# Kernel tuning notes

Measured on AMD Instinct MI355X. Metric: run time of the kernel, lower is better.

The kernel has to match this reference:

```python
import jax, jax.numpy as jnp
import numpy as np

B, D, H, W, Q = 16, 768, 64, 64, 128


def setup_inputs() -> dict:
    key = jax.random.key(0)
    ks = jax.random.split(key, 6)
    s = 0.02  # param init scale
    return {
        "visual_feat": jax.random.normal(ks[0], (B, D, H, W), jnp.float32),
        "text_feat": jax.random.normal(ks[1], (B, Q, D), jnp.float32),
        "Wq": jax.random.normal(ks[2], (D, D), jnp.float32) * s,
        "bq": jnp.zeros((D,), jnp.float32),
        "Wk": jax.random.normal(ks[3], (D, D), jnp.float32) * s,
        "bk": jnp.zeros((D,), jnp.float32),
        "Wv": jax.random.normal(ks[4], (D, D), jnp.float32) * s,
        "bv": jnp.zeros((D,), jnp.float32),
    }


def _entropy_weights(x):
    # x: [B, T, D] -> softmax over features, per-token entropy, softmax over tokens -> [B, T]
    p = jax.nn.softmax(x, axis=-1)
    ent = -jnp.sum(p * jnp.log(p + 1e-9), axis=-1)
    return jax.nn.softmax(ent, axis=-1)


def reference(visual_feat, text_feat, Wq, bq, Wk, bk, Wv, bv):
    b, d, h, w = visual_feat.shape
    vf = visual_feat.reshape(b, d, h * w).transpose(0, 2, 1)  # [B, N, D]
    ve = _entropy_weights(vf)          # [B, N]
    te = _entropy_weights(text_feat)   # [B, Q]
    q = vf @ Wq.T + bq                 # [B, N, D]
    k = text_feat @ Wk.T + bk          # [B, Q, D]
    v = text_feat @ Wv.T + bv          # [B, Q, D]
    attn = jnp.einsum('bnd,bqd->bnq', q, k) / jnp.sqrt(jnp.float32(d))
    attn = attn * (ve[:, :, None] * te[:, None, :])  # entropy outer-product modulation
    attn = jax.nn.softmax(attn, axis=-1)
    enhanced = jnp.einsum('bnq,bqd->bnd', attn, v)   # [B, N, D]
    return enhanced.transpose(0, 2, 1).reshape(b, d, h, w)
```

## Files before the change

kernel.cpp:

```cpp
#include <hip/hip_runtime.h>

#define B_ 16
#define D_ 768
#define N_ 4096
#define Q_ 128

typedef __attribute__((ext_vector_type(4))) float f32x4;
typedef __attribute__((ext_vector_type(8))) short short8;
typedef __attribute__((ext_vector_type(4))) short sv4;

__device__ __forceinline__ unsigned short f2bf(float f) {
  union { float f; unsigned u; } x; x.f = f;
  unsigned u = x.u;
  unsigned r = u + 0x7fffu + ((u >> 16) & 1u);
  return (unsigned short)(r >> 16);
}
__device__ __forceinline__ float bf2f(unsigned short h) {
  union { unsigned u; float f; } x; x.u = ((unsigned)h) << 16;
  return x.f;
}

__global__ __launch_bounds__(256) void cast_bf16_kernel(
    const float* __restrict__ src, unsigned short* __restrict__ dst, int n4) {
  int i = blockIdx.x * 256 + threadIdx.x;
  if (i >= n4) return;
  float4 v = ((const float4*)src)[i];
  ushort4 o;
  o.x = f2bf(v.x); o.y = f2bf(v.y); o.z = f2bf(v.z); o.w = f2bf(v.w);
  ((ushort4*)dst)[i] = o;
}

__global__ __launch_bounds__(256) void transpose_cast_kernel(
    const float* __restrict__ src, unsigned short* __restrict__ dst, int rows, int cols) {
  __shared__ float tile[32][33];
  int bx = blockIdx.x * 32, by = blockIdx.y * 32;
  int tx = threadIdx.x & 31, ty = threadIdx.x >> 5;
  #pragma unroll
  for (int i = 0; i < 32; i += 8)
    tile[ty + i][tx] = src[(size_t)(by + ty + i) * cols + bx + tx];
  __syncthreads();
  #pragma unroll
  for (int i = 0; i < 32; i += 8)
    dst[(size_t)(bx + ty + i) * rows + by + tx] = f2bf(tile[tx][ty + i]);
}

__global__ __launch_bounds__(256) void row_entropy_kernel(
    const float* __restrict__ X, float* __restrict__ ent, int K) {
  int row = blockIdx.x * 4 + (threadIdx.x >> 6);
  int lane = threadIdx.x & 63;
  const float* x = X + (size_t)row * K;
  float m = -__builtin_inff(), s = 0.f, t = 0.f;
  for (int k = lane; k < K; k += 64) {
    float v = x[k];
    float nm = fmaxf(m, v);
    float c = __expf(m - nm);
    float e = __expf(v - nm);
    s = s * c + e;
    t = t * c + v * e;
    m = nm;
  }
  #pragma unroll
  for (int off = 32; off > 0; off >>= 1) {
    float m2 = __shfl_xor(m, off);
    float s2 = __shfl_xor(s, off);
    float t2 = __shfl_xor(t, off);
    float nm = fmaxf(m, m2);
    float c1 = __expf(m - nm), c2 = __expf(m2 - nm);
    s = s * c1 + s2 * c2;
    t = t * c1 + t2 * c2;
    m = nm;
  }
  if (lane == 0) ent[row] = m + __logf(s) - t / s;
}

__global__ __launch_bounds__(256) void visual_entropy_kernel(
    const float* __restrict__ vis, float* __restrict__ ent) {
  int bb = blockIdx.x >> 6;
  int n0 = (blockIdx.x & 63) * 64;
  int t = threadIdx.x;
  int tok = t & 63;
  int slice = t >> 6;
  const float* base = vis + (size_t)bb * D_ * N_ + (size_t)slice * 192 * N_ + n0 + tok;
  float m = -__builtin_inff(), s = 0.f, tt = 0.f;
  for (int d = 0; d < 192; d++) {
    float v = base[(size_t)d * N_];
    float nm = fmaxf(m, v);
    float c = __expf(m - nm);
    float e = __expf(v - nm);
    s = s * c + e; tt = tt * c + v * e; m = nm;
  }
  __shared__ float sm[256], ss[256], st[256];
  sm[t] = m; ss[t] = s; st[t] = tt;
  __syncthreads();
  if (t < 64) {
    #pragma unroll
    for (int k = 1; k < 4; k++) {
      float m2 = sm[t + 64 * k], s2 = ss[t + 64 * k], t2 = st[t + 64 * k];
      float nm = fmaxf(m, m2);
      float c1 = __expf(m - nm), c2 = __expf(m2 - nm);
      s = s * c1 + s2 * c2; tt = tt * c1 + t2 * c2; m = nm;
    }
    ent[(size_t)bb * N_ + n0 + t] = m + __logf(s) - tt / s;
  }
}

__global__ __launch_bounds__(128) void softmax128_kernel(
    const float* __restrict__ ent, float* __restrict__ w) {
  int b = blockIdx.x, t = threadIdx.x;
  float v = ent[b * 128 + t];
  float m = v;
  #pragma unroll
  for (int off = 32; off; off >>= 1) m = fmaxf(m, __shfl_xor(m, off));
  __shared__ float sm2[2], ssum[2];
  int wv = t >> 6;
  if ((t & 63) == 0) sm2[wv] = m;
  __syncthreads();
  m = fmaxf(sm2[0], sm2[1]);
  float e = __expf(v - m);
  float s = e;
  #pragma unroll
  for (int off = 32; off; off >>= 1) s += __shfl_xor(s, off);
  if ((t & 63) == 0) ssum[wv] = s;
  __syncthreads();
  s = ssum[0] + ssum[1];
  w[b * 128 + t] = e / s;
}

__global__ __launch_bounds__(1024) void softmax4096_kernel(
    const float* __restrict__ ent, float* __restrict__ w) {
  int b = blockIdx.x, t = threadIdx.x;
  const float* e = ent + (size_t)b * N_;
  float v[4];
  float m = -__builtin_inff();
  #pragma unroll
  for (int i = 0; i < 4; i++) { v[i] = e[t + 1024 * i]; m = fmaxf(m, v[i]); }
  #pragma unroll
  for (int off = 32; off; off >>= 1) m = fmaxf(m, __shfl_xor(m, off));
  __shared__ float red[16];
  int wv = t >> 6;
  if ((t & 63) == 0) red[wv] = m;
  __syncthreads();
  if (t < 16) {
    float x = red[t];
    #pragma unroll
    for (int off = 8; off; off >>= 1) x = fmaxf(x, __shfl_xor(x, off));
    red[t] = x;
  }
  __syncthreads();
  m = red[0];
  float ev[4];
  float s = 0.f;
  #pragma unroll
  for (int i = 0; i < 4; i++) { ev[i] = __expf(v[i] - m); s += ev[i]; }
  #pragma unroll
  for (int off = 32; off; off >>= 1) s += __shfl_xor(s, off);
  __syncthreads();
  if ((t & 63) == 0) red[wv] = s;
  __syncthreads();
  if (t < 16) {
    float x = red[t];
    #pragma unroll
    for (int off = 8; off; off >>= 1) x += __shfl_xor(x, off);
    red[t] = x;
  }
  __syncthreads();
  s = red[0];
  #pragma unroll
  for (int i = 0; i < 4; i++) w[(size_t)b * N_ + t + 1024 * i] = ev[i] / s;
}

template <int MODE>
__global__ __launch_bounds__(256) void gemm_nt_kernel(
    const unsigned short* __restrict__ A, const unsigned short* __restrict__ Bm,
    const float* __restrict__ bias, unsigned short* __restrict__ C) {
  constexpr int LDA = 40;
  __shared__ unsigned short As[64 * LDA];
  __shared__ unsigned short Bs[64 * LDA];
  int m0 = blockIdx.x * 64, n0 = blockIdx.y * 64;
  int t = threadIdx.x, wave = t >> 6, lane = t & 63;
  int wm = (wave & 1) * 32, wn = (wave >> 1) * 32;
  int fl = lane & 15, fq = lane >> 4;
  f32x4 acc[2][2];
  #pragma unroll
  for (int i = 0; i < 2; i++)
    #pragma unroll
    for (int j = 0; j < 2; j++) acc[i][j] = {0.f, 0.f, 0.f, 0.f};
  int sr = t >> 2, sc = (t & 3) * 8;
  for (int k0 = 0; k0 < D_; k0 += 32) {
    uint4 av = *(const uint4*)(A + (size_t)(m0 + sr) * D_ + k0 + sc);
    uint4 bv = *(const uint4*)(Bm + (size_t)(n0 + sr) * D_ + k0 + sc);
    __syncthreads();
    *(uint4*)(As + sr * LDA + sc) = av;
    *(uint4*)(Bs + sr * LDA + sc) = bv;
    __syncthreads();
    short8 afr[2], bfr[2];
    #pragma unroll
    for (int i = 0; i < 2; i++)
      afr[i] = *(const short8*)(As + (wm + i * 16 + fl) * LDA + fq * 8);
    #pragma unroll
    for (int j = 0; j < 2; j++)
      bfr[j] = *(const short8*)(Bs + (wn + j * 16 + fl) * LDA + fq * 8);
    #pragma unroll
    for (int i = 0; i < 2; i++)
      #pragma unroll
      for (int j = 0; j < 2; j++)
        acc[i][j] = __builtin_amdgcn_mfma_f32_16x16x32_bf16(afr[i], bfr[j], acc[i][j], 0, 0, 0);
  }
  #pragma unroll
  for (int i = 0; i < 2; i++)
    #pragma unroll
    for (int j = 0; j < 2; j++) {
      int n = n0 + wn + j * 16 + fl;
      float bb = (MODE >= 1) ? bias[n] : 0.f;
      #pragma unroll
      for (int r = 0; r < 4; r++) {
        int m = m0 + wm + i * 16 + fq * 4 + r;
        float val = acc[i][j][r] + bb;
        if (MODE == 2) {
          int bt = m >> 7, q = m & 127;
          C[((size_t)bt * D_ + n) * Q_ + q] = f2bf(val);
        } else {
          C[(size_t)m * D_ + n] = f2bf(val);
        }
      }
    }
}

__global__ __launch_bounds__(256) void bias_dot_kernel(
    const unsigned short* __restrict__ kb, const float* __restrict__ bq,
    float* __restrict__ skq) {
  int row = blockIdx.x * 4 + (threadIdx.x >> 6);
  int lane = threadIdx.x & 63;
  const unsigned short* kr = kb + (size_t)row * D_;
  float s = 0.f;
  for (int k = lane; k < D_; k += 64) s += bq[k] * bf2f(kr[k]);
  #pragma unroll
  for (int off = 32; off; off >>= 1) s += __shfl_xor(s, off);
  if (lane == 0) skq[row] = s;
}

__global__ __launch_bounds__(256, 2) void attn_main_kernel(
    const float* __restrict__ vis,
    const unsigned short* __restrict__ kq,
    const unsigned short* __restrict__ vT,
    const float* __restrict__ ve,
    const float* __restrict__ te,
    const float* __restrict__ skq,
    float* __restrict__ out)
{
  constexpr int LA = 68;
  constexpr int LB = 72;
  constexpr int LP = 136;
  __shared__ unsigned short region0[30464];
  __shared__ float stats[2][128][2];
  unsigned short* As = region0;
  unsigned short* Bs = region0 + 8704;
  unsigned short* Ps = region0;
  unsigned short* Vs = region0 + 17408;

  const int bb = blockIdx.x >> 5;
  const int n0 = (blockIdx.x & 31) * 128;
  const int t = threadIdx.x;
  const int wave = t >> 6, lane = t & 63;
  const int fl = lane & 15, fq = lane >> 4;
  const int wm = (wave & 1) * 64;
  const int wq = (wave >> 1) * 64;

  const float* abase = vis + (size_t)bb * D_ * N_ + n0;
  const unsigned short* bbase = kq + (size_t)bb * Q_ * D_;

  f32x4 acc[4][4];
  #pragma unroll
  for (int i = 0; i < 4; i++)
    #pragma unroll
    for (int j = 0; j < 4; j++) acc[i][j] = {0.f, 0.f, 0.f, 0.f};

  const int smi = t & 127;
  const int ph = t >> 7;

  for (int k0 = 0; k0 < D_; k0 += 64) {
    __syncthreads();
    #pragma unroll
    for (int i = 0; i < 16; i++) {
      const int kk = 2 * (ph + 2 * i);
      const float v0 = abase[(size_t)(k0 + kk) * N_ + smi];
      const float v1 = abase[(size_t)(k0 + kk + 1) * N_ + smi];
      const unsigned pk = (unsigned)f2bf(v0) | ((unsigned)f2bf(v1) << 16);
      *(unsigned*)(As + smi * LA + kk) = pk;
    }
    #pragma unroll
    for (int i = 0; i < 4; i++) {
      const int c = t + 256 * i;
      const int q = c >> 3, kc = (c & 7) * 8;
      const uint4 v = *(const uint4*)(bbase + (size_t)q * D_ + k0 + kc);
      *(uint4*)(Bs + q * LB + kc) = v;
    }
    __syncthreads();
    #pragma unroll
    for (int ks = 0; ks < 2; ks++) {
      short8 afr[4], bfr[4];
      #pragma unroll
      for (int i = 0; i < 4; i++) {
        const unsigned short* pa = As + (wm + i * 16 + fl) * LA + ks * 32 + fq * 8;
        sv4 lo = *(const sv4*)pa;
        sv4 hi = *(const sv4*)(pa + 4);
        afr[i] = __builtin_shufflevector(lo, hi, 0, 1, 2, 3, 4, 5, 6, 7);
      }
      #pragma unroll
      for (int j = 0; j < 4; j++)
        bfr[j] = *(const short8*)(Bs + (wq + j * 16 + fl) * LB + ks * 32 + fq * 8);
      #pragma unroll
      for (int i = 0; i < 4; i++)
        #pragma unroll
        for (int j = 0; j < 4; j++)
          acc[i][j] = __builtin_amdgcn_mfma_f32_16x16x32_bf16(afr[i], bfr[j], acc[i][j], 0, 0, 0);
    }
  }

  const float rsD = 0.03608439182435161f;
  float tev[4], skv[4];
  #pragma unroll
  for (int j = 0; j < 4; j++) {
    int q = wq + j * 16 + fl;
    tev[j] = te[bb * Q_ + q];
    skv[j] = skq[bb * Q_ + q];
  }
  float vev4[4][4];
  #pragma unroll
  for (int i = 0; i < 4; i++)
    #pragma unroll
    for (int r = 0; r < 4; r++)
      vev4[i][r] = ve[(size_t)bb * N_ + n0 + wm + i * 16 + fq * 4 + r];

  float rmax[4][4], rsum[4][4];
  #pragma unroll
  for (int i = 0; i < 4; i++)
    #pragma unroll
    for (int r = 0; r < 4; r++) rmax[i][r] = -__builtin_inff();
  #pragma unroll
  for (int i = 0; i < 4; i++)
    #pragma unroll
    for (int j = 0; j < 4; j++)
      #pragma unroll
      for (int r = 0; r < 4; r++) {
        float L = (acc[i][j][r] + skv[j]) * rsD * vev4[i][r] * tev[j];
        acc[i][j][r] = L;
        rmax[i][r] = fmaxf(rmax[i][r], L);
      }
  #pragma unroll
  for (int off = 1; off < 16; off <<= 1)
    #pragma unroll
    for (int i = 0; i < 4; i++)
      #pragma unroll
      for (int r = 0; r < 4; r++)
        rmax[i][r] = fmaxf(rmax[i][r], __shfl_xor(rmax[i][r], off));
  #pragma unroll
  for (int i = 0; i < 4; i++)
    #pragma unroll
    for (int r = 0; r < 4; r++) rsum[i][r] = 0.f;
  #pragma unroll
  for (int i = 0; i < 4; i++)
    #pragma unroll
    for (int j = 0; j < 4; j++)
      #pragma unroll
      for (int r = 0; r < 4; r++) {
        float e = __expf(acc[i][j][r] - rmax[i][r]);
        acc[i][j][r] = e;
        rsum[i][r] += e;
      }
  #pragma unroll
  for (int off = 1; off < 16; off <<= 1)
    #pragma unroll
    for (int i = 0; i < 4; i++)
      #pragma unroll
      for (int r = 0; r < 4; r++) rsum[i][r] += __shfl_xor(rsum[i][r], off);

  const int qh = wq >> 6;
  if (fl == 0) {
    #pragma unroll
    for (int i = 0; i < 4; i++)
      #pragma unroll
      for (int r = 0; r < 4; r++) {
        int m = wm + i * 16 + fq * 4 + r;
        stats[qh][m][0] = rmax[i][r];
        stats[qh][m][1] = rsum[i][r];
      }
  }
  __syncthreads();
  float fac[4][4];
  #pragma unroll
  for (int i = 0; i < 4; i++)
    #pragma unroll
    for (int r = 0; r < 4; r++) {
      int m = wm + i * 16 + fq * 4 + r;
      float M2 = stats[1 - qh][m][0], S2 = stats[1 - qh][m][1];
      float Mf = fmaxf(rmax[i][r], M2);
      float sf = rsum[i][r] * __expf(rmax[i][r] - Mf) + S2 * __expf(M2 - Mf);
      fac[i][r] = __expf(rmax[i][r] - Mf) / sf;
    }
  #pragma unroll
  for (int i = 0; i < 4; i++)
    #pragma unroll
    for (int j = 0; j < 4; j++)
      #pragma unroll
      for (int r = 0; r < 4; r++) {
        int m = wm + i * 16 + fq * 4 + r;
        int q = wq + j * 16 + fl;
        Ps[m * LP + q] = f2bf(acc[i][j][r] * fac[i][r]);
      }

  const int wd = (wave & 1) * 48;
  const int wm2 = (wave >> 1) * 64;
  for (int dc = 0; dc < 8; dc++) {
    __syncthreads();
    const unsigned short* vbase = vT + ((size_t)bb * D_ + dc * 96) * Q_;
    #pragma unroll
    for (int i = 0; i < 6; i++) {
      const int c = t + 256 * i;
      const int d = c >> 4, qc = (c & 15) * 8;
      const uint4 v = *(const uint4*)(vbase + (size_t)d * Q_ + qc);
      *(uint4*)(Vs + d * LP + qc) = v;
    }
    __syncthreads();
    f32x4 acc2[3][4];
    #pragma unroll
    for (int i = 0; i < 3; i++)
      #pragma unroll
      for (int j = 0; j < 4; j++) acc2[i][j] = {0.f, 0.f, 0.f, 0.f};
    #pragma unroll
    for (int ks = 0; ks < 4; ks++) {
      short8 vfr[3], pfr[4];
      #pragma unroll
      for (int i = 0; i < 3; i++)
        vfr[i] = *(const short8*)(Vs + (wd + i * 16 + fl) * LP + ks * 32 + fq * 8);
      #pragma unroll
      for (int j = 0; j < 4; j++)
        pfr[j] = *(const short8*)(Ps + (wm2 + j * 16 + fl) * LP + ks * 32 + fq * 8);
      #pragma unroll
      for (int i = 0; i < 3; i++)
        #pragma unroll
        for (int j = 0; j < 4; j++)
          acc2[i][j] = __builtin_amdgcn_mfma_f32_16x16x32_bf16(vfr[i], pfr[j], acc2[i][j], 0, 0, 0);
    }
    float* obase = out + ((size_t)bb * D_ + dc * 96) * N_ + n0;
    #pragma unroll
    for (int i = 0; i < 3; i++)
      #pragma unroll
      for (int j = 0; j < 4; j++) {
        int mm = wm2 + j * 16 + fl;
        #pragma unroll
        for (int r = 0; r < 4; r++) {
          int d = wd + i * 16 + fq * 4 + r;
          obase[(size_t)d * N_ + mm] = acc2[i][j][r];
        }
      }
  }
}

extern "C" void kernel_launch(void* const* d_in, const int* in_sizes, int n_in,
                              void* d_out, int out_size, void* d_ws, size_t ws_size,
                              hipStream_t stream) {
  const float* vis  = (const float*)d_in[0];
  const float* text = (const float*)d_in[1];
  const float* Wq   = (const float*)d_in[2];
  const float* bq   = (const float*)d_in[3];
  const float* Wk   = (const float*)d_in[4];
  const float* bk   = (const float*)d_in[5];
  const float* Wv   = (const float*)d_in[6];
  const float* bv   = (const float*)d_in[7];
  float* out = (float*)d_out;
  char* ws = (char*)d_ws;

  unsigned short* textb = (unsigned short*)(ws + 0);
  unsigned short* Wkb   = (unsigned short*)(ws + 3145728);
  unsigned short* Wvb   = (unsigned short*)(ws + 4325376);
  unsigned short* WqTb  = (unsigned short*)(ws + 5505024);
  unsigned short* kb    = (unsigned short*)(ws + 6684672);
  unsigned short* kqb   = (unsigned short*)(ws + 9830400);
  unsigned short* vTb   = (unsigned short*)(ws + 12976128);
  float* ent_t = (float*)(ws + 16121856);
  float* tew   = (float*)(ws + 16130048);
  float* ent_v = (float*)(ws + 16138240);
  float* vew   = (float*)(ws + 16400384);
  float* skq   = (float*)(ws + 16662528);

  cast_bf16_kernel<<<1536, 256, 0, stream>>>(text, textb, 2048 * 768 / 4);
  cast_bf16_kernel<<<576, 256, 0, stream>>>(Wk, Wkb, 768 * 768 / 4);
  cast_bf16_kernel<<<576, 256, 0, stream>>>(Wv, Wvb, 768 * 768 / 4);
  transpose_cast_kernel<<<dim3(24, 24), 256, 0, stream>>>(Wq, WqTb, 768, 768);

  row_entropy_kernel<<<512, 256, 0, stream>>>(text, ent_t, 768);
  softmax128_kernel<<<16, 128, 0, stream>>>(ent_t, tew);
  visual_entropy_kernel<<<1024, 256, 0, stream>>>(vis, ent_v);
  softmax4096_kernel<<<16, 1024, 0, stream>>>(ent_v, vew);

  gemm_nt_kernel<1><<<dim3(32, 12), 256, 0, stream>>>(textb, Wkb, bk, kb);
  gemm_nt_kernel<2><<<dim3(32, 12), 256, 0, stream>>>(textb, Wvb, bv, vTb);
  gemm_nt_kernel<0><<<dim3(32, 12), 256, 0, stream>>>(kb, WqTb, nullptr, kqb);
  bias_dot_kernel<<<512, 256, 0, stream>>>(kb, bq, skq);

  attn_main_kernel<<<512, 256, 0, stream>>>(vis, kqb, vTb, vew, tew, skq, out);
}
```

Baseline: 463.3 us.

## Fuse entropy passes with bf16 casts, precombine Wq/Wk, stage visual as bf16

Several preparation steps are reorganised. The Wq and Wk projections are folded into one precomputed weight product, so the text side needs a single GEMM, and the bias terms are handled by small vector-matrix kernels. Text entropy, the bf16 cast and the bias dot product are merged into one kernel. When the workspace is large enough, a new pass computes the visual entropy while writing a token-major bf16 copy of the visual features, which the attention kernel then loads with contiguous vector reads instead of strided fp32 reads. The entropy code also drops the running-max subtraction (unsafe for large inputs), the small GEMM uses a K step of 64, and the bf16 copy adds extra write and read traffic.

```diff
diff --git a/kernel.cpp b/kernel.cpp
--- a/kernel.cpp
+++ b/kernel.cpp
@@ -20,57 +20,159 @@
   return x.f;
 }
 
-__global__ __launch_bounds__(256) void cast_bf16_kernel(
-    const float* __restrict__ src, unsigned short* __restrict__ dst, int n4) {
-  int i = blockIdx.x * 256 + threadIdx.x;
-  if (i >= n4) return;
-  float4 v = ((const float4*)src)[i];
-  ushort4 o;
-  o.x = f2bf(v.x); o.y = f2bf(v.y); o.z = f2bf(v.z); o.w = f2bf(v.w);
-  ((ushort4*)dst)[i] = o;
-}
-
-__global__ __launch_bounds__(256) void transpose_cast_kernel(
-    const float* __restrict__ src, unsigned short* __restrict__ dst, int rows, int cols) {
+__global__ __launch_bounds__(256) void weights_prep_kernel(
+    const float* __restrict__ Wv, const float* __restrict__ Wq,
+    const float* __restrict__ Wk,
+    unsigned short* __restrict__ Wvb, unsigned short* __restrict__ WqTb,
+    unsigned short* __restrict__ WkTb) {
   __shared__ float tile[32][33];
-  int bx = blockIdx.x * 32, by = blockIdx.y * 32;
-  int tx = threadIdx.x & 31, ty = threadIdx.x >> 5;
-  #pragma unroll
-  for (int i = 0; i < 32; i += 8)
-    tile[ty + i][tx] = src[(size_t)(by + ty + i) * cols + bx + tx];
-  __syncthreads();
-  #pragma unroll
-  for (int i = 0; i < 32; i += 8)
-    dst[(size_t)(bx + ty + i) * rows + by + tx] = f2bf(tile[tx][ty + i]);
-}
-
-__global__ __launch_bounds__(256) void row_entropy_kernel(
-    const float* __restrict__ X, float* __restrict__ ent, int K) {
+  const int z = blockIdx.z;
+  if (z == 0) {
+    int i = (blockIdx.y * 24 + blockIdx.x) * 256 + threadIdx.x;
+    float4 v = ((const float4*)Wv)[i];
+    ushort4 o;
+    o.x = f2bf(v.x); o.y = f2bf(v.y); o.z = f2bf(v.z); o.w = f2bf(v.w);
+    ((ushort4*)Wvb)[i] = o;
+  } else {
+    const float* src = (z == 1) ? Wq : Wk;
+    unsigned short* dst = (z == 1) ? WqTb : WkTb;
+    int bx = blockIdx.x * 32, by = blockIdx.y * 32;
+    int tx = threadIdx.x & 31, ty = threadIdx.x >> 5;
+    #pragma unroll
+    for (int i = 0; i < 32; i += 8)
+      tile[ty + i][tx] = src[(size_t)(by + ty + i) * D_ + bx + tx];
+    __syncthreads();
+    #pragma unroll
+    for (int i = 0; i < 32; i += 8)
+      dst[(size_t)(bx + ty + i) * D_ + by + tx] = f2bf(tile[tx][ty + i]);
+  }
+}
+
+__global__ __launch_bounds__(256) void vecmat_kernel(
+    const float* __restrict__ Wk, const float* __restrict__ Wq,
+    const float* __restrict__ bq, const float* __restrict__ bk,
+    float* __restrict__ wkbq, float* __restrict__ bias2, float* __restrict__ bqbk) {
+  const int y = blockIdx.y, t = threadIdx.x;
+  if (y == 2) {
+    if (blockIdx.x != 0) return;
+    float s = 0.f;
+    for (int k = t; k < D_; k += 256) s += bq[k] * bk[k];
+    #pragma unroll
+    for (int off = 32; off; off >>= 1) s += __shfl_xor(s, off);
+    __shared__ float red[4];
+    if ((t & 63) == 0) red[t >> 6] = s;
+    __syncthreads();
+    if (t == 0) bqbk[0] = red[0] + red[1] + red[2] + red[3];
+    return;
+  }
+  const float* M = y ? Wq : Wk;
+  const float* vec = y ? bk : bq;
+  float* outp = y ? bias2 : wkbq;
+  const int col = blockIdx.x * 256 + t;
+  float s = 0.f;
+  #pragma unroll 4
+  for (int n = 0; n < D_; n++) s += M[(size_t)n * D_ + col] * vec[n];
+  outp[col] = s;
+}
+
+__global__ __launch_bounds__(256) void text_prep_kernel(
+    const float* __restrict__ text, unsigned short* __restrict__ textb,
+    float* __restrict__ ent, const float* __restrict__ wkbq,
+    const float* __restrict__ bqbk, float* __restrict__ skq) {
   int row = blockIdx.x * 4 + (threadIdx.x >> 6);
   int lane = threadIdx.x & 63;
-  const float* x = X + (size_t)row * K;
-  float m = -__builtin_inff(), s = 0.f, t = 0.f;
-  for (int k = lane; k < K; k += 64) {
-    float v = x[k];
-    float nm = fmaxf(m, v);
-    float c = __expf(m - nm);
-    float e = __expf(v - nm);
-    s = s * c + e;
-    t = t * c + v * e;
-    m = nm;
-  }
-  #pragma unroll
-  for (int off = 32; off > 0; off >>= 1) {
-    float m2 = __shfl_xor(m, off);
-    float s2 = __shfl_xor(s, off);
-    float t2 = __shfl_xor(t, off);
-    float nm = fmaxf(m, m2);
-    float c1 = __expf(m - nm), c2 = __expf(m2 - nm);
-    s = s * c1 + s2 * c2;
-    t = t * c1 + t2 * c2;
-    m = nm;
-  }
-  if (lane == 0) ent[row] = m + __logf(s) - t / s;
+  const float4* src = (const float4*)(text + (size_t)row * D_);
+  const float4* w4p = (const float4*)wkbq;
+  ushort4* dst = (ushort4*)(textb + (size_t)row * D_);
+  float s = 0.f, tt = 0.f, s2 = 0.f;
+  #pragma unroll
+  for (int j = 0; j < 3; j++) {
+    float4 v = src[lane + 64 * j];
+    float4 w = w4p[lane + 64 * j];
+    float e0 = __expf(v.x), e1 = __expf(v.y), e2 = __expf(v.z), e3 = __expf(v.w);
+    s += (e0 + e1) + (e2 + e3);
+    tt += v.x * e0 + v.y * e1;
+    tt += v.z * e2 + v.w * e3;
+    s2 += v.x * w.x + v.y * w.y + v.z * w.z + v.w * w.w;
+    ushort4 o;
+    o.x = f2bf(v.x); o.y = f2bf(v.y); o.z = f2bf(v.z); o.w = f2bf(v.w);
+    dst[lane + 64 * j] = o;
+  }
+  #pragma unroll
+  for (int off = 32; off; off >>= 1) {
+    s += __shfl_xor(s, off);
+    tt += __shfl_xor(tt, off);
+    s2 += __shfl_xor(s2, off);
+  }
+  if (lane == 0) {
+    ent[row] = __logf(s) - tt / s;
+    skq[row] = s2 + bqbk[0];
+  }
+}
+
+__global__ __launch_bounds__(128) void softmax128_kernel(
+    const float* __restrict__ ent, float* __restrict__ w) {
+  int b = blockIdx.x, t = threadIdx.x;
+  float v = ent[b * 128 + t];
+  float m = v;
+  #pragma unroll
+  for (int off = 32; off; off >>= 1) m = fmaxf(m, __shfl_xor(m, off));
+  __shared__ float sm2[2], ssum[2];
+  int wv = t >> 6;
+  if ((t & 63) == 0) sm2[wv] = m;
+  __syncthreads();
+  m = fmaxf(sm2[0], sm2[1]);
+  float e = __expf(v - m);
+  float s = e;
+  #pragma unroll
+  for (int off = 32; off; off >>= 1) s += __shfl_xor(s, off);
+  if ((t & 63) == 0) ssum[wv] = s;
+  __syncthreads();
+  s = ssum[0] + ssum[1];
+  w[b * 128 + t] = e / s;
+}
+
+__global__ __launch_bounds__(1024) void softmax4096_kernel(
+    const float* __restrict__ ent, float* __restrict__ w) {
+  int b = blockIdx.x, t = threadIdx.x;
+  const float* e = ent + (size_t)b * N_;
+  float v[4];
+  float m = -__builtin_inff();
+  #pragma unroll
+  for (int i = 0; i < 4; i++) { v[i] = e[t + 1024 * i]; m = fmaxf(m, v[i]); }
+  #pragma unroll
+  for (int off = 32; off; off >>= 1) m = fmaxf(m, __shfl_xor(m, off));
+  __shared__ float red[16];
+  int wv = t >> 6;
+  if ((t & 63) == 0) red[wv] = m;
+  __syncthreads();
+  if (t < 16) {
+    float x = red[t];
+    #pragma unroll
+    for (int off = 8; off; off >>= 1) x = fmaxf(x, __shfl_xor(x, off));
+    red[t] = x;
+  }
+  __syncthreads();
+  m = red[0];
+  float ev[4];
+  float s = 0.f;
+  #pragma unroll
+  for (int i = 0; i < 4; i++) { ev[i] = __expf(v[i] - m); s += ev[i]; }
+  #pragma unroll
+  for (int off = 32; off; off >>= 1) s += __shfl_xor(s, off);
+  __syncthreads();
+  if ((t & 63) == 0) red[wv] = s;
+  __syncthreads();
+  if (t < 16) {
+    float x = red[t];
+    #pragma unroll
+    for (int off = 8; off; off >>= 1) x += __shfl_xor(x, off);
+    red[t] = x;
+  }
+  __syncthreads();
+  s = red[0];
+  #pragma unroll
+  for (int i = 0; i < 4; i++) w[(size_t)b * N_ + t + 1024 * i] = ev[i] / s;
 }
 
 __global__ __launch_bounds__(256) void visual_entropy_kernel(
@@ -104,76 +206,55 @@
   }
 }
 
-__global__ __launch_bounds__(128) void softmax128_kernel(
-    const float* __restrict__ ent, float* __restrict__ w) {
-  int b = blockIdx.x, t = threadIdx.x;
-  float v = ent[b * 128 + t];
-  float m = v;
-  #pragma unroll
-  for (int off = 32; off; off >>= 1) m = fmaxf(m, __shfl_xor(m, off));
-  __shared__ float sm2[2], ssum[2];
-  int wv = t >> 6;
-  if ((t & 63) == 0) sm2[wv] = m;
-  __syncthreads();
-  m = fmaxf(sm2[0], sm2[1]);
-  float e = __expf(v - m);
-  float s = e;
-  #pragma unroll
-  for (int off = 32; off; off >>= 1) s += __shfl_xor(s, off);
-  if ((t & 63) == 0) ssum[wv] = s;
-  __syncthreads();
-  s = ssum[0] + ssum[1];
-  w[b * 128 + t] = e / s;
-}
-
-__global__ __launch_bounds__(1024) void softmax4096_kernel(
-    const float* __restrict__ ent, float* __restrict__ w) {
-  int b = blockIdx.x, t = threadIdx.x;
-  const float* e = ent + (size_t)b * N_;
-  float v[4];
-  float m = -__builtin_inff();
-  #pragma unroll
-  for (int i = 0; i < 4; i++) { v[i] = e[t + 1024 * i]; m = fmaxf(m, v[i]); }
-  #pragma unroll
-  for (int off = 32; off; off >>= 1) m = fmaxf(m, __shfl_xor(m, off));
-  __shared__ float red[16];
-  int wv = t >> 6;
-  if ((t & 63) == 0) red[wv] = m;
-  __syncthreads();
-  if (t < 16) {
-    float x = red[t];
-    #pragma unroll
-    for (int off = 8; off; off >>= 1) x = fmaxf(x, __shfl_xor(x, off));
-    red[t] = x;
-  }
-  __syncthreads();
-  m = red[0];
-  float ev[4];
-  float s = 0.f;
-  #pragma unroll
-  for (int i = 0; i < 4; i++) { ev[i] = __expf(v[i] - m); s += ev[i]; }
-  #pragma unroll
-  for (int off = 32; off; off >>= 1) s += __shfl_xor(s, off);
-  __syncthreads();
-  if ((t & 63) == 0) red[wv] = s;
-  __syncthreads();
-  if (t < 16) {
-    float x = red[t];
-    #pragma unroll
-    for (int off = 8; off; off >>= 1) x += __shfl_xor(x, off);
-    red[t] = x;
-  }
-  __syncthreads();
-  s = red[0];
-  #pragma unroll
-  for (int i = 0; i < 4; i++) w[(size_t)b * N_ + t + 1024 * i] = ev[i] / s;
+__global__ __launch_bounds__(256) void vis_prep_kernel(
+    const float* __restrict__ vis, unsigned short* __restrict__ visb,
+    float* __restrict__ ent) {
+  constexpr int LA = 68;
+  __shared__ unsigned short As[128 * LA];
+  __shared__ float2 esh[256];
+  const int bb = blockIdx.x >> 5;
+  const int n0 = (blockIdx.x & 31) * 128;
+  const int t = threadIdx.x;
+  const int smi = t & 127;
+  const int ph = t >> 7;
+  const float* abase = vis + (size_t)bb * D_ * N_ + n0;
+  unsigned short* obase = visb + ((size_t)bb * N_ + n0) * D_;
+  float es = 0.f, ets = 0.f;
+  for (int k0 = 0; k0 < D_; k0 += 64) {
+    __syncthreads();
+    #pragma unroll
+    for (int i = 0; i < 16; i++) {
+      const int kk = 2 * (ph + 2 * i);
+      const float v0 = abase[(size_t)(k0 + kk) * N_ + smi];
+      const float v1 = abase[(size_t)(k0 + kk + 1) * N_ + smi];
+      const float e0 = __expf(v0), e1 = __expf(v1);
+      es += e0 + e1;
+      ets += v0 * e0 + v1 * e1;
+      const unsigned pk = (unsigned)f2bf(v0) | ((unsigned)f2bf(v1) << 16);
+      *(unsigned*)(As + smi * LA + kk) = pk;
+    }
+    __syncthreads();
+    #pragma unroll
+    for (int i = 0; i < 8; i++) {
+      const int c = t + 256 * i;
+      const int n = c >> 4, m = c & 15;
+      *(uint2*)(obase + (size_t)n * D_ + k0 + m * 4) = *(const uint2*)(As + n * LA + m * 4);
+    }
+  }
+  esh[t] = {es, ets};
+  __syncthreads();
+  if (t < 128) {
+    const float S = es + esh[t + 128].x;
+    const float T = ets + esh[t + 128].y;
+    ent[(size_t)bb * N_ + n0 + t] = __logf(S) - T / S;
+  }
 }
 
 template <int MODE>
 __global__ __launch_bounds__(256) void gemm_nt_kernel(
     const unsigned short* __restrict__ A, const unsigned short* __restrict__ Bm,
     const float* __restrict__ bias, unsigned short* __restrict__ C) {
-  constexpr int LDA = 40;
+  constexpr int LDA = 72;
   __shared__ unsigned short As[64 * LDA];
   __shared__ unsigned short Bs[64 * LDA];
   int m0 = blockIdx.x * 64, n0 = blockIdx.y * 64;
@@ -185,26 +266,31 @@
   for (int i = 0; i < 2; i++)
     #pragma unroll
     for (int j = 0; j < 2; j++) acc[i][j] = {0.f, 0.f, 0.f, 0.f};
-  int sr = t >> 2, sc = (t & 3) * 8;
-  for (int k0 = 0; k0 < D_; k0 += 32) {
-    uint4 av = *(const uint4*)(A + (size_t)(m0 + sr) * D_ + k0 + sc);
-    uint4 bv = *(const uint4*)(Bm + (size_t)(n0 + sr) * D_ + k0 + sc);
-    __syncthreads();
-    *(uint4*)(As + sr * LDA + sc) = av;
-    *(uint4*)(Bs + sr * LDA + sc) = bv;
-    __syncthreads();
-    short8 afr[2], bfr[2];
-    #pragma unroll
-    for (int i = 0; i < 2; i++)
-      afr[i] = *(const short8*)(As + (wm + i * 16 + fl) * LDA + fq * 8);
-    #pragma unroll
-    for (int j = 0; j < 2; j++)
-      bfr[j] = *(const short8*)(Bs + (wn + j * 16 + fl) * LDA + fq * 8);
-    #pragma unroll
-    for (int i = 0; i < 2; i++)
+  for (int k0 = 0; k0 < D_; k0 += 64) {
+    __syncthreads();
+    #pragma unroll
+    for (int i = 0; i < 2; i++) {
+      int c = t + 256 * i;
+      int sr = c >> 3, sc = (c & 7) * 8;
+      *(uint4*)(As + sr * LDA + sc) = *(const uint4*)(A + (size_t)(m0 + sr) * D_ + k0 + sc);
+      *(uint4*)(Bs + sr * LDA + sc) = *(const uint4*)(Bm + (size_t)(n0 + sr) * D_ + k0 + sc);
+    }
+    __syncthreads();
+    #pragma unroll
+    for (int ks = 0; ks < 2; ks++) {
+      short8 afr[2], bfr[2];
+      #pragma unroll
+      for (int i = 0; i < 2; i++)
+        afr[i] = *(const short8*)(As + (wm + i * 16 + fl) * LDA + ks * 32 + fq * 8);
       #pragma unroll
       for (int j = 0; j < 2; j++)
-        acc[i][j] = __builtin_amdgcn_mfma_f32_16x16x32_bf16(afr[i], bfr[j], acc[i][j], 0, 0, 0);
+        bfr[j] = *(const short8*)(Bs + (wn + j * 16 + fl) * LDA + ks * 32 + fq * 8);
+      #pragma unroll
+      for (int i = 0; i < 2; i++)
+        #pragma unroll
+        for (int j = 0; j < 2; j++)
+          acc[i][j] = __builtin_amdgcn_mfma_f32_16x16x32_bf16(afr[i], bfr[j], acc[i][j], 0, 0, 0);
+    }
   }
   #pragma unroll
   for (int i = 0; i < 2; i++)
@@ -226,21 +312,10 @@
     }
 }
 
-__global__ __launch_bounds__(256) void bias_dot_kernel(
-    const unsigned short* __restrict__ kb, const float* __restrict__ bq,
-    float* __restrict__ skq) {
-  int row = blockIdx.x * 4 + (threadIdx.x >> 6);
-  int lane = threadIdx.x & 63;
-  const unsigned short* kr = kb + (size_t)row * D_;
-  float s = 0.f;
-  for (int k = lane; k < D_; k += 64) s += bq[k] * bf2f(kr[k]);
-  #pragma unroll
-  for (int off = 32; off; off >>= 1) s += __shfl_xor(s, off);
-  if (lane == 0) skq[row] = s;
-}
-
+template <int ASRC>
 __global__ __launch_bounds__(256, 2) void attn_main_kernel(
     const float* __restrict__ vis,
+    const unsigned short* __restrict__ visb,
     const unsigned short* __restrict__ kq,
     const unsigned short* __restrict__ vT,
     const float* __restrict__ ve,
@@ -267,6 +342,7 @@
   const int wq = (wave >> 1) * 64;
 
   const float* abase = vis + (size_t)bb * D_ * N_ + n0;
+  const unsigned short* vbrow = visb + ((size_t)bb * N_ + n0) * D_;
   const unsigned short* bbase = kq + (size_t)bb * Q_ * D_;
 
   f32x4 acc[4][4];
@@ -280,13 +356,24 @@
 
   for (int k0 = 0; k0 < D_; k0 += 64) {
     __syncthreads();
-    #pragma unroll
-    for (int i = 0; i < 16; i++) {
-      const int kk = 2 * (ph + 2 * i);
-      const float v0 = abase[(size_t)(k0 + kk) * N_ + smi];
-      const float v1 = abase[(size_t)(k0 + kk + 1) * N_ + smi];
-      const unsigned pk = (unsigned)f2bf(v0) | ((unsigned)f2bf(v1) << 16);
-      *(unsigned*)(As + smi * LA + kk) = pk;
+    if (ASRC == 1) {
+      #pragma unroll
+      for (int i = 0; i < 4; i++) {
+        const int c = t + 256 * i;
+        const int n = c >> 3, j = c & 7;
+        const uint4 v = *(const uint4*)(vbrow + (size_t)n * D_ + k0 + j * 8);
+        *(uint2*)(As + n * LA + j * 8) = {v.x, v.y};
+        *(uint2*)(As + n * LA + j * 8 + 4) = {v.z, v.w};
+      }
+    } else {
+      #pragma unroll
+      for (int i = 0; i < 16; i++) {
+        const int kk = 2 * (ph + 2 * i);
+        const float v0 = abase[(size_t)(k0 + kk) * N_ + smi];
+        const float v1 = abase[(size_t)(k0 + kk + 1) * N_ + smi];
+        const unsigned pk = (unsigned)f2bf(v0) | ((unsigned)f2bf(v1) << 16);
+        *(unsigned*)(As + smi * LA + kk) = pk;
+      }
     }
     #pragma unroll
     for (int i = 0; i < 4; i++) {
@@ -472,10 +559,13 @@
   char* ws = (char*)d_ws;
 
   unsigned short* textb = (unsigned short*)(ws + 0);
-  unsigned short* Wkb   = (unsigned short*)(ws + 3145728);
+  unsigned short* WkTb  = (unsigned short*)(ws + 3145728);
   unsigned short* Wvb   = (unsigned short*)(ws + 4325376);
   unsigned short* WqTb  = (unsigned short*)(ws + 5505024);
-  unsigned short* kb    = (unsigned short*)(ws + 6684672);
+  unsigned short* W2Tb  = (unsigned short*)(ws + 6684672);
+  float* wkbq  = (float*)(ws + 7864320);
+  float* bias2 = (float*)(ws + 7867392);
+  float* bqbk  = (float*)(ws + 7870464);
   unsigned short* kqb   = (unsigned short*)(ws + 9830400);
   unsigned short* vTb   = (unsigned short*)(ws + 12976128);
   float* ent_t = (float*)(ws + 16121856);
@@ -483,21 +573,25 @@
   float* ent_v = (float*)(ws + 16138240);
   float* vew   = (float*)(ws + 16400384);
   float* skq   = (float*)(ws + 16662528);
-
-  cast_bf16_kernel<<<1536, 256, 0, stream>>>(text, textb, 2048 * 768 / 4);
-  cast_bf16_kernel<<<576, 256, 0, stream>>>(Wk, Wkb, 768 * 768 / 4);
-  cast_bf16_kernel<<<576, 256, 0, stream>>>(Wv, Wvb, 768 * 768 / 4);
-  transpose_cast_kernel<<<dim3(24, 24), 256, 0, stream>>>(Wq, WqTb, 768, 768);
-
-  row_entropy_kernel<<<512, 256, 0, stream>>>(text, ent_t, 768);
+  unsigned short* visb = (unsigned short*)(ws + 16777216);
+  const bool big = ws_size >= (size_t)16777216 + (size_t)100663296;
+
+  weights_prep_kernel<<<dim3(24, 24, 3), 256, 0, stream>>>(Wv, Wq, Wk, Wvb, WqTb, WkTb);
+  vecmat_kernel<<<dim3(3, 3), 256, 0, stream>>>(Wk, Wq, bq, bk, wkbq, bias2, bqbk);
+  text_prep_kernel<<<512, 256, 0, stream>>>(text, textb, ent_t, wkbq, bqbk, skq);
   softmax128_kernel<<<16, 128, 0, stream>>>(ent_t, tew);
-  visual_entropy_kernel<<<1024, 256, 0, stream>>>(vis, ent_v);
-  softmax4096_kernel<<<16, 1024, 0, stream>>>(ent_v, vew);
-
-  gemm_nt_kernel<1><<<dim3(32, 12), 256, 0, stream>>>(textb, Wkb, bk, kb);
+
+  gemm_nt_kernel<0><<<dim3(12, 12), 256, 0, stream>>>(WqTb, WkTb, nullptr, W2Tb);
+  gemm_nt_kernel<1><<<dim3(32, 12), 256, 0, stream>>>(textb, W2Tb, bias2, kqb);
   gemm_nt_kernel<2><<<dim3(32, 12), 256, 0, stream>>>(textb, Wvb, bv, vTb);
-  gemm_nt_kernel<0><<<dim3(32, 12), 256, 0, stream>>>(kb, WqTb, nullptr, kqb);
-  bias_dot_kernel<<<512, 256, 0, stream>>>(kb, bq, skq);
-
-  attn_main_kernel<<<512, 256, 0, stream>>>(vis, kqb, vTb, vew, tew, skq, out);
-}
+
+  if (big) {
+    vis_prep_kernel<<<512, 256, 0, stream>>>(vis, visb, ent_v);
+    softmax4096_kernel<<<16, 1024, 0, stream>>>(ent_v, vew);
+    attn_main_kernel<1><<<512, 256, 0, stream>>>(vis, visb, kqb, vTb, vew, tew, skq, out);
+  } else {
+    visual_entropy_kernel<<<1024, 256, 0, stream>>>(vis, ent_v);
+    softmax4096_kernel<<<16, 1024, 0, stream>>>(ent_v, vew);
+    attn_main_kernel<0><<<512, 256, 0, stream>>>(vis, visb, kqb, vTb, vew, tew, skq, out);
+  }
+}
```

Result: slower. 547.2 us (+18.1%).
